# Performance work log

Measured on AMD Instinct MI355X. Metric: run time of the kernel, lower is better.

## Reference

```python
import jax, jax.numpy as jnp
import numpy as np

SPATIAL_SHAPES = np.array([[128, 128], [64, 64], [32, 32], [16, 16]], dtype=np.int32)  # (H, W) per level
D_MODEL = 256
D_FFN = 1024
N_LEVELS = 4
N_HEADS = 8
N_POINTS = 4
HEAD_DIM = D_MODEL // N_HEADS
B = 2
LEN = int((SPATIAL_SHAPES[:, 0] * SPATIAL_SHAPES[:, 1]).sum())  # 21760


def layer_norm(x, g, b, eps=1e-5):
    mu = x.mean(-1, keepdims=True)
    var = ((x - mu) ** 2).mean(-1, keepdims=True)
    return (x - mu) / jnp.sqrt(var + eps) * g + b


def ms_deform_attn_core(value, sampling_locations, attention_weights):
    # value: [B, Len, M, D]; locations: [B, Lq, M, L, P, 2] in [0,1]; weights: [B, Lq, M, L, P]
    B_, _, M, D = value.shape
    Lq = sampling_locations.shape[1]
    P = sampling_locations.shape[4]
    out = jnp.zeros((B_, M, Lq, D), value.dtype)
    start = 0
    for lvl, (H, W) in enumerate(SPATIAL_SHAPES.tolist()):
        v = value[:, start:start + H * W].transpose(0, 2, 1, 3)  # [B, M, H*W, D]
        start += H * W
        loc = sampling_locations[:, :, :, lvl].transpose(0, 2, 1, 3, 4)  # [B, M, Lq, P, 2]
        # grid_sample semantics: align_corners=False, padding_mode='zeros'
        x = loc[..., 0] * W - 0.5
        y = loc[..., 1] * H - 0.5
        x0 = jnp.floor(x)
        y0 = jnp.floor(y)
        wx = (x - x0)[..., None]
        wy = (y - y0)[..., None]

        def gather(xi, yi):
            valid = ((xi >= 0) & (xi < W) & (yi >= 0) & (yi < H)).astype(value.dtype)
            idx = (jnp.clip(yi, 0, H - 1) * W + jnp.clip(xi, 0, W - 1)).astype(jnp.int32)
            idx = idx.reshape(B_, M, Lq * P)
            g = jnp.take_along_axis(v, idx[..., None], axis=2).reshape(B_, M, Lq, P, D)
            return g * valid[..., None]

        v00 = gather(x0, y0)
        v01 = gather(x0 + 1, y0)
        v10 = gather(x0, y0 + 1)
        v11 = gather(x0 + 1, y0 + 1)
        samp = (v00 * (1 - wx) + v01 * wx) * (1 - wy) + (v10 * (1 - wx) + v11 * wx) * wy
        w_l = attention_weights[:, :, :, lvl].transpose(0, 2, 1, 3)  # [B, M, Lq, P]
        out = out + (samp * w_l[..., None]).sum(axis=3)
    return out.transpose(0, 2, 1, 3).reshape(B_, Lq, M * D)


def setup_inputs() -> dict:
    key = jax.random.key(0)
    ks = jax.random.split(key, 16)
    f32 = jnp.float32

    def lin(k, fan_in, fan_out, scale=None):
        s = scale if scale is not None else 1.0 / np.sqrt(fan_in)
        return jax.random.normal(k, (fan_in, fan_out), f32) * s

    starts = np.concatenate([[0], np.cumsum(SPATIAL_SHAPES[:, 0] * SPATIAL_SHAPES[:, 1])[:-1]]).astype(np.int32)
    inp = {
        "src": jax.random.normal(ks[0], (B, LEN, D_MODEL), f32),
        "pos": jax.random.normal(ks[1], (B, LEN, D_MODEL), f32),
        "reference_points": jax.random.uniform(ks[2], (B, LEN, N_LEVELS, 2), f32),
        "spatial_shapes": jnp.asarray(SPATIAL_SHAPES),
        "level_start_index": jnp.asarray(starts),
        "norm1_g": jnp.ones((D_MODEL,), f32), "norm1_b": jnp.zeros((D_MODEL,), f32),
        "norm2_g": jnp.ones((D_MODEL,), f32), "norm2_b": jnp.zeros((D_MODEL,), f32),
        "W_value": lin(ks[3], D_MODEL, D_MODEL), "b_value": jnp.zeros((D_MODEL,), f32),
        "W_off": lin(ks[4], D_MODEL, N_HEADS * N_LEVELS * N_POINTS * 2, scale=0.01),
        "b_off": jax.random.normal(ks[5], (N_HEADS * N_LEVELS * N_POINTS * 2,), f32) * 0.01,
        "W_attn": lin(ks[6], D_MODEL, N_HEADS * N_LEVELS * N_POINTS),
        "b_attn": jnp.zeros((N_HEADS * N_LEVELS * N_POINTS,), f32),
        "W_out": lin(ks[7], D_MODEL, D_MODEL), "b_out": jnp.zeros((D_MODEL,), f32),
        "W_ffn1": lin(ks[8], D_MODEL, D_FFN), "b_ffn1": jnp.zeros((D_FFN,), f32),
        "W_ffn2": lin(ks[9], D_FFN, D_MODEL), "b_ffn2": jnp.zeros((D_MODEL,), f32),
    }
    return inp


def reference(src, pos, reference_points, spatial_shapes, level_start_index,
              norm1_g, norm1_b, norm2_g, norm2_b,
              W_value, b_value, W_off, b_off, W_attn, b_attn, W_out, b_out,
              W_ffn1, b_ffn1, W_ffn2, b_ffn2):
    B_, Lq, C = src.shape
    # pre-norm deformable self-attention; NOTE: value path uses un-normed src (faithful to source)
    q = layer_norm(src, norm1_g, norm1_b) + pos
    value = (src @ W_value + b_value).reshape(B_, Lq, N_HEADS, HEAD_DIM)
    offsets = (q @ W_off + b_off).reshape(B_, Lq, N_HEADS, N_LEVELS, N_POINTS, 2)
    attn = jax.nn.softmax((q @ W_attn + b_attn).reshape(B_, Lq, N_HEADS, N_LEVELS * N_POINTS), axis=-1)
    attn = attn.reshape(B_, Lq, N_HEADS, N_LEVELS, N_POINTS)
    offset_normalizer = spatial_shapes[..., ::-1].astype(src.dtype)  # (W, H) per level
    loc = reference_points[:, :, None, :, None, :] + offsets / offset_normalizer[None, None, None, :, None, :]
    attn_out = ms_deform_attn_core(value, loc, attn) @ W_out + b_out
    src = src + attn_out
    h = layer_norm(src, norm2_g, norm2_b)
    h = jax.nn.gelu(h @ W_ffn1 + b_ffn1, approximate=False) @ W_ffn2 + b_ffn2
    return src + h
```

## Files before the change

kernel.cpp:

```cpp
#include <hip/hip_runtime.h>
#include <hip/hip_bf16.h>
#include <math.h>

#define LEN_TOT 21760
#define BATCH 2
#define MROWS (BATCH * LEN_TOT)
#define DMODEL 256
#define DFFN 1024

typedef unsigned short ushort_t;
typedef __attribute__((ext_vector_type(8))) short short8;
typedef __attribute__((ext_vector_type(4))) float floatx4;
typedef __attribute__((address_space(3))) ushort_t lds_us;
typedef __attribute__((address_space(1))) const ushort_t glb_us;

__device__ __forceinline__ ushort_t f2b(float f) {
    unsigned u = __float_as_uint(f);
    unsigned r = (u + 0x7FFFu + ((u >> 16) & 1u)) >> 16;
    return (ushort_t)r;
}

struct TP {
    const float* s[6];
    ushort_t*    d[6];
    int K[6];
    int N[6];
    int start[7];
};

__global__ __launch_bounds__(256) void transpose_convert(TP tp) {
    __shared__ float tile[32][33];
    int blk = blockIdx.x;
    int seg = 0;
    while (seg < 5 && blk >= tp.start[seg + 1]) seg++;
    int local = blk - tp.start[seg];
    int K = tp.K[seg], N = tp.N[seg];
    int tn = N >> 5;
    int k0 = (local / tn) << 5, n0 = (local % tn) << 5;
    int r = threadIdx.x >> 5, c = threadIdx.x & 31;
    const float* src = tp.s[seg];
    #pragma unroll
    for (int rr = r; rr < 32; rr += 8)
        tile[rr][c] = src[(size_t)(k0 + rr) * N + n0 + c];
    __syncthreads();
    ushort_t* dst = tp.d[seg];
    #pragma unroll
    for (int rr = r; rr < 32; rr += 8)
        dst[(size_t)(n0 + rr) * K + k0 + c] = f2b(tile[c][rr]);
}

__global__ __launch_bounds__(256) void ln_dual_kernel(
    const float* __restrict__ x, const float* __restrict__ g,
    const float* __restrict__ bb, const float* __restrict__ addv,
    ushort_t* __restrict__ y_bf, ushort_t* __restrict__ x_bf)
{
    int row  = blockIdx.x * 4 + (threadIdx.x >> 6);
    int lane = threadIdx.x & 63;
    size_t base = (size_t)row * DMODEL + lane * 4;
    float4 v = *(const float4*)(x + base);

    float s = v.x + v.y + v.z + v.w;
    #pragma unroll
    for (int o = 32; o; o >>= 1) s += __shfl_xor(s, o, 64);
    float mu = s * (1.0f / 256.0f);

    float d0 = v.x - mu, d1 = v.y - mu, d2 = v.z - mu, d3 = v.w - mu;
    float vs = d0*d0 + d1*d1 + d2*d2 + d3*d3;
    #pragma unroll
    for (int o = 32; o; o >>= 1) vs += __shfl_xor(vs, o, 64);
    float rstd = rsqrtf(vs * (1.0f / 256.0f) + 1e-5f);

    float4 gv = *(const float4*)(g  + lane * 4);
    float4 bv = *(const float4*)(bb + lane * 4);
    float o0 = d0 * rstd * gv.x + bv.x;
    float o1 = d1 * rstd * gv.y + bv.y;
    float o2 = d2 * rstd * gv.z + bv.z;
    float o3 = d3 * rstd * gv.w + bv.w;
    if (addv) {
        float4 av = *(const float4*)(addv + base);
        o0 += av.x; o1 += av.y; o2 += av.z; o3 += av.w;
    }
    ushort4 ob = {f2b(o0), f2b(o1), f2b(o2), f2b(o3)};
    *(ushort4*)(y_bf + base) = ob;
    if (x_bf) {
        ushort4 xb = {f2b(v.x), f2b(v.y), f2b(v.z), f2b(v.w)};
        *(ushort4*)(x_bf + base) = xb;
    }
}

template<int GELU_ACT, int HAS_RES, int OUT_BF16>
__global__ __launch_bounds__(256) void gemm_mfma(
    const ushort_t* __restrict__ A, const ushort_t* __restrict__ Bt,
    const float* __restrict__ bias, const float* __restrict__ res,
    float* __restrict__ C, ushort_t* __restrict__ Cbf,
    int M, int N, int K)
{
    constexpr int BM = 128, BK = 32;
    __shared__ __align__(16) ushort_t As[BM * BK];
    __shared__ __align__(16) ushort_t Bs[BM * BK];

    const int tid  = threadIdx.x;
    const int wave = tid >> 6;
    const int lane = tid & 63;
    const int wm = (wave & 1) * 64;
    const int wn = (wave >> 1) * 64;
    const int ml = lane & 15;
    const int quad = lane >> 4;
    const int m0 = blockIdx.y * BM, n0 = blockIdx.x * BM;

    const int r0 = tid >> 2, s0 = tid & 3;
    const int r1 = (tid + 256) >> 2;

    floatx4 acc[4][4] = {};

    for (int k0 = 0; k0 < K; k0 += BK) {
        const ushort_t* gA0 = A  + (size_t)(m0 + r0) * K + k0 + s0 * 8;
        const ushort_t* gA1 = A  + (size_t)(m0 + r1) * K + k0 + s0 * 8;
        const ushort_t* gB0 = Bt + (size_t)(n0 + r0) * K + k0 + s0 * 8;
        const ushort_t* gB1 = Bt + (size_t)(n0 + r1) * K + k0 + s0 * 8;
        __builtin_amdgcn_global_load_lds((glb_us*)gA0, (lds_us*)(As + tid * 8),        16, 0, 0);
        __builtin_amdgcn_global_load_lds((glb_us*)gA1, (lds_us*)(As + (tid + 256) * 8),16, 0, 0);
        __builtin_amdgcn_global_load_lds((glb_us*)gB0, (lds_us*)(Bs + tid * 8),        16, 0, 0);
        __builtin_amdgcn_global_load_lds((glb_us*)gB1, (lds_us*)(Bs + (tid + 256) * 8),16, 0, 0);
        __syncthreads();

        short8 af[4], bfr[4];
        #pragma unroll
        for (int i = 0; i < 4; i++)
            af[i] = *(const short8*)(As + (wm + i * 16 + ml) * BK + quad * 8);
        #pragma unroll
        for (int j = 0; j < 4; j++)
            bfr[j] = *(const short8*)(Bs + (wn + j * 16 + ml) * BK + quad * 8);
        #pragma unroll
        for (int i = 0; i < 4; i++)
            #pragma unroll
            for (int j = 0; j < 4; j++)
                acc[i][j] = __builtin_amdgcn_mfma_f32_16x16x32_bf16(
                    af[i], bfr[j], acc[i][j], 0, 0, 0);
        __syncthreads();
    }

    if (OUT_BF16) {
        ushort_t* pool  = (wave < 2) ? As : Bs;
        ushort_t* wbase = pool + (wave & 1) * 2048;
        const int lr  = lane >> 2;
        const int sg  = lane & 3;
        #pragma unroll
        for (int i = 0; i < 4; i++) {
            ushort_t* wbuf = wbase + (i & 1) * 1024;
            #pragma unroll
            for (int j = 0; j < 4; j++) {
                float bc = bias[n0 + wn + j * 16 + ml];
                #pragma unroll
                for (int r = 0; r < 4; r++) {
                    float v = acc[i][j][r] + bc;
                    if (GELU_ACT) v = 0.5f * v * (1.0f + erff(v * 0.7071067811865476f));
                    if (HAS_RES)
                        v += res[(size_t)(m0 + wm + i * 16 + quad * 4 + r) * N
                                 + n0 + wn + j * 16 + ml];
                    wbuf[(quad * 4 + r) * 64 + j * 16 + ml] = f2b(v);
                }
            }
            asm volatile("s_waitcnt lgkmcnt(0)" ::: "memory");
            #pragma unroll
            for (int h = 0; h < 2; h++) {
                short8 vv = *(const short8*)(wbuf + lr * 64 + (sg + 4 * h) * 8);
                *(short8*)(Cbf + (size_t)(m0 + wm + i * 16 + lr) * N
                                 + n0 + wn + (sg + 4 * h) * 8) = vv;
            }
        }
    } else {
        #pragma unroll
        for (int j = 0; j < 4; j++) {
            int col = n0 + wn + j * 16 + ml;
            float bc = bias[col];
            #pragma unroll
            for (int i = 0; i < 4; i++) {
                int row = m0 + wm + i * 16 + quad * 4;
                #pragma unroll
                for (int r = 0; r < 4; r++) {
                    float v = acc[i][j][r] + bc;
                    if (GELU_ACT) v = 0.5f * v * (1.0f + erff(v * 0.7071067811865476f));
                    if (HAS_RES) v += res[(size_t)(row + r) * N + col];
                    C[(size_t)(row + r) * N + col] = v;
                }
            }
        }
    }
}

__global__ __launch_bounds__(256) void msdeform_kernel(
    const float* __restrict__ value, const float* __restrict__ offs,
    const float* __restrict__ logits, const float* __restrict__ refp,
    ushort_t* __restrict__ out_bf)
{
    int gid = blockIdx.x * 8 + (threadIdx.x >> 5);
    int l   = threadIdx.x & 31;
    int bq  = gid >> 3;
    int m   = gid & 7;
    int b   = (bq >= LEN_TOT) ? 1 : 0;

    int i = l & 15;
    float logit = logits[(size_t)gid * 16 + i];
    float mx = logit;
    #pragma unroll
    for (int o = 8; o; o >>= 1) mx = fmaxf(mx, __shfl_xor(mx, o, 32));
    float e = __expf(logit - mx);
    float se = e;
    #pragma unroll
    for (int o = 8; o; o >>= 1) se += __shfl_xor(se, o, 32);
    float prob = e / se;

    int lvl = i >> 2;
    int Wl  = 128 >> lvl;
    float Wf = (float)Wl;
    const int ST_[4] = {0, 16384, 20480, 21504};

    float2 off2 = ((const float2*)offs)[(size_t)gid * 16 + i];
    float2 ref2 = ((const float2*)refp)[(size_t)bq * 4 + lvl];
    float xs = fmaf(ref2.x, Wf, off2.x) - 0.5f;
    float ys = fmaf(ref2.y, Wf, off2.y) - 0.5f;
    float xf = floorf(xs), yf = floorf(ys);
    int x0 = (int)xf, y0 = (int)yf;
    float wx = xs - xf, wy = ys - yf;
    float wx1 = 1.0f - wx, wy1 = 1.0f - wy;

    bool vx0 = (x0 >= 0) & (x0 < Wl);
    bool vx1 = (x0 + 1 >= 0) & (x0 + 1 < Wl);
    bool vy0 = (y0 >= 0) & (y0 < Wl);
    bool vy1 = (y0 + 1 >= 0) & (y0 + 1 < Wl);
    int cx0 = min(max(x0, 0), Wl - 1);
    int cx1 = min(max(x0 + 1, 0), Wl - 1);
    int cy0 = min(max(y0, 0), Wl - 1);
    int cy1 = min(max(y0 + 1, 0), Wl - 1);

    int vbase = b * LEN_TOT + ST_[lvl];
    int i00 = (vbase + cy0 * Wl + cx0) * 256 + m * 32;
    int i01 = (vbase + cy0 * Wl + cx1) * 256 + m * 32;
    int i10 = (vbase + cy1 * Wl + cx0) * 256 + m * 32;
    int i11 = (vbase + cy1 * Wl + cx1) * 256 + m * 32;
    float w00 = (vx0 && vy0) ? prob * wx1 * wy1 : 0.0f;
    float w01 = (vx1 && vy0) ? prob * wx  * wy1 : 0.0f;
    float w10 = (vx0 && vy1) ? prob * wx1 * wy  : 0.0f;
    float w11 = (vx1 && vy1) ? prob * wx  * wy  : 0.0f;

    int sA = l >> 2;
    int cA = l & 3;
    int t0 = __shfl(i00, sA, 32), t1 = __shfl(i01, sA, 32);
    int t2 = __shfl(i10, sA, 32), t3 = __shfl(i11, sA, 32);
    int addrA = (cA == 0) ? t0 : (cA == 1) ? t1 : (cA == 2) ? t2 : t3;
    float u0 = __shfl(w00, sA, 32), u1 = __shfl(w01, sA, 32);
    float u2 = __shfl(w10, sA, 32), u3 = __shfl(w11, sA, 32);
    float wA = (cA == 0) ? u0 : (cA == 1) ? u1 : (cA == 2) ? u2 : u3;
    t0 = __shfl(i00, sA + 8, 32); t1 = __shfl(i01, sA + 8, 32);
    t2 = __shfl(i10, sA + 8, 32); t3 = __shfl(i11, sA + 8, 32);
    int addrB = (cA == 0) ? t0 : (cA == 1) ? t1 : (cA == 2) ? t2 : t3;
    u0 = __shfl(w00, sA + 8, 32); u1 = __shfl(w01, sA + 8, 32);
    u2 = __shfl(w10, sA + 8, 32); u3 = __shfl(w11, sA + 8, 32);
    float wB = (cA == 0) ? u0 : (cA == 1) ? u1 : (cA == 2) ? u2 : u3;

    int cl = l >> 3;
    int d4 = l & 7;
    float ax = 0.0f, ay = 0.0f, az = 0.0f, aw = 0.0f;
    #pragma unroll
    for (int s = 0; s < 8; s++) {
        int   a = __shfl(addrA, s * 4 + cl, 32);
        float w = __shfl(wA,    s * 4 + cl, 32);
        float4 v = *(const float4*)(value + a + (d4 << 2));
        ax = fmaf(w, v.x, ax); ay = fmaf(w, v.y, ay);
        az = fmaf(w, v.z, az); aw = fmaf(w, v.w, aw);
    }
    #pragma unroll
    for (int s = 0; s < 8; s++) {
        int   a = __shfl(addrB, s * 4 + cl, 32);
        float w = __shfl(wB,    s * 4 + cl, 32);
        float4 v = *(const float4*)(value + a + (d4 << 2));
        ax = fmaf(w, v.x, ax); ay = fmaf(w, v.y, ay);
        az = fmaf(w, v.z, az); aw = fmaf(w, v.w, aw);
    }
    ax += __shfl_xor(ax, 8, 32);  ay += __shfl_xor(ay, 8, 32);
    az += __shfl_xor(az, 8, 32);  aw += __shfl_xor(aw, 8, 32);
    ax += __shfl_xor(ax, 16, 32); ay += __shfl_xor(ay, 16, 32);
    az += __shfl_xor(az, 16, 32); aw += __shfl_xor(aw, 16, 32);

    if (l < 8) {
        ushort4 o = {f2b(ax), f2b(ay), f2b(az), f2b(aw)};
        *(ushort4*)(out_bf + (size_t)gid * 32 + (d4 << 2)) = o;
    }
}

extern "C" void kernel_launch(void* const* d_in, const int* in_sizes, int n_in,
                              void* d_out, int out_size, void* d_ws, size_t ws_size,
                              hipStream_t stream)
{
    const float* src  = (const float*)d_in[0];
    const float* pos  = (const float*)d_in[1];
    const float* refp = (const float*)d_in[2];
    const float* n1g = (const float*)d_in[5];
    const float* n1b = (const float*)d_in[6];
    const float* n2g = (const float*)d_in[7];
    const float* n2b = (const float*)d_in[8];
    const float* Wv  = (const float*)d_in[9];
    const float* bv  = (const float*)d_in[10];
    const float* Wof = (const float*)d_in[11];
    const float* bof = (const float*)d_in[12];
    const float* Wat = (const float*)d_in[13];
    const float* bat = (const float*)d_in[14];
    const float* Wo  = (const float*)d_in[15];
    const float* bo  = (const float*)d_in[16];
    const float* Wf1 = (const float*)d_in[17];
    const float* bf1 = (const float*)d_in[18];
    const float* Wf2 = (const float*)d_in[19];
    const float* bf2 = (const float*)d_in[20];
    float* out = (float*)d_out;

    char* ws = (char*)d_ws;
    const int M = MROWS;
    const size_t SZ_BF = (size_t)M * 256 * 2;
    const size_t SZ_F  = (size_t)M * 256 * 4;

    ushort_t* q_bf    = (ushort_t*)(ws);
    float*    value   = (float*)   (ws + SZ_BF);
    ushort_t* src_bf  = (ushort_t*)(ws + SZ_BF + SZ_F);
    float*    offsb   = (float*)   (ws + 2 * SZ_BF + SZ_F);
    float*    logitsb = (float*)   (ws + 2 * SZ_BF + 2 * SZ_F);
    ushort_t* h0_bf   = q_bf;
    ushort_t* sampled = src_bf;
    float*    src2    = value;
    ushort_t* h1_bf   = src_bf;
    char* wtp = ws + 2 * SZ_BF + 2 * SZ_F + (size_t)M * 128 * 4;
    ushort_t* WvT  = (ushort_t*)(wtp);
    ushort_t* WofT = WvT  + 256 * 256;
    ushort_t* WatT = WofT + 256 * 256;
    ushort_t* WoT  = WatT + 256 * 128;
    ushort_t* Wf1T = WoT  + 256 * 256;
    ushort_t* Wf2T = Wf1T + 256 * 1024;

    TP tp;
    tp.s[0] = Wv;  tp.d[0] = WvT;  tp.K[0] = 256;  tp.N[0] = 256;
    tp.s[1] = Wof; tp.d[1] = WofT; tp.K[1] = 256;  tp.N[1] = 256;
    tp.s[2] = Wat; tp.d[2] = WatT; tp.K[2] = 256;  tp.N[2] = 128;
    tp.s[3] = Wo;  tp.d[3] = WoT;  tp.K[3] = 256;  tp.N[3] = 256;
    tp.s[4] = Wf1; tp.d[4] = Wf1T; tp.K[4] = 256;  tp.N[4] = 1024;
    tp.s[5] = Wf2; tp.d[5] = Wf2T; tp.K[5] = 1024; tp.N[5] = 256;
    tp.start[0] = 0;   tp.start[1] = 64;  tp.start[2] = 128;
    tp.start[3] = 160; tp.start[4] = 224; tp.start[5] = 480; tp.start[6] = 736;
    transpose_convert<<<736, 256, 0, stream>>>(tp);

    ln_dual_kernel<<<M / 4, 256, 0, stream>>>(src, n1g, n1b, pos, q_bf, src_bf);
    gemm_mfma<0, 0, 0><<<dim3(2, M / 128), 256, 0, stream>>>(
        src_bf, WvT, bv, nullptr, value, nullptr, M, 256, 256);
    gemm_mfma<0, 0, 0><<<dim3(2, M / 128), 256, 0, stream>>>(
        q_bf, WofT, bof, nullptr, offsb, nullptr, M, 256, 256);
    gemm_mfma<0, 0, 0><<<dim3(1, M / 128), 256, 0, stream>>>(
        q_bf, WatT, bat, nullptr, logitsb, nullptr, M, 128, 256);
    msdeform_kernel<<<M, 256, 0, stream>>>(value, offsb, logitsb, refp, sampled);
    gemm_mfma<0, 1, 0><<<dim3(2, M / 128), 256, 0, stream>>>(
        sampled, WoT, bo, src, src2, nullptr, M, 256, 256);
    ln_dual_kernel<<<M / 4, 256, 0, stream>>>(src2, n2g, n2b, nullptr, h0_bf, nullptr);
    gemm_mfma<1, 0, 1><<<dim3(8, M / 128), 256, 0, stream>>>(
        h0_bf, Wf1T, bf1, nullptr, nullptr, h1_bf, M, 1024, 256);
    gemm_mfma<0, 1, 0><<<dim3(2, M / 128), 256, 0, stream>>>(
        h1_bf, Wf2T, bf2, src2, out, nullptr, M, 256, 1024);
}
```

Baseline: 505.1 us.

## Use bf16 value, fuse offset/attn GEMMs, swizzle BK=64 GEMM, chunk FFN

The GEMM K-tile grows to 64, with an XOR-swizzled LDS layout meant to avoid bank conflicts. The value projection now writes bf16, and msdeform gathers bf16, which halves gather bandwidth. Offset and attention-logit GEMMs merge into one N=384 GEMM with concatenated biases. msdeform is restructured to one query per block, with sampling metadata staged in shared memory. The FFN runs in two row chunks so the intermediate buffer is smaller and more cache-friendly, at the cost of extra launches and bf16 rounding of the value tensor.

```diff
diff --git a/kernel.cpp b/kernel.cpp
--- a/kernel.cpp
+++ b/kernel.cpp
@@ -49,6 +49,12 @@
         dst[(size_t)(n0 + rr) * K + k0 + c] = f2b(tile[c][rr]);
 }
 
+__global__ void bias_cat(const float* __restrict__ a, const float* __restrict__ b,
+                         float* __restrict__ o) {
+    int t = threadIdx.x;
+    o[t] = (t < 256) ? a[t] : b[t - 256];
+}
+
 __global__ __launch_bounds__(256) void ln_dual_kernel(
     const float* __restrict__ x, const float* __restrict__ g,
     const float* __restrict__ bb, const float* __restrict__ addv,
@@ -95,7 +101,7 @@
     float* __restrict__ C, ushort_t* __restrict__ Cbf,
     int M, int N, int K)
 {
-    constexpr int BM = 128, BK = 32;
+    constexpr int BM = 128, BK = 64;
     __shared__ __align__(16) ushort_t As[BM * BK];
     __shared__ __align__(16) ushort_t Bs[BM * BK];
 
@@ -107,36 +113,42 @@
     const int ml = lane & 15;
     const int quad = lane >> 4;
     const int m0 = blockIdx.y * BM, n0 = blockIdx.x * BM;
-
-    const int r0 = tid >> 2, s0 = tid & 3;
-    const int r1 = (tid + 256) >> 2;
+    const int swz = ml & 7;
 
     floatx4 acc[4][4] = {};
 
     for (int k0 = 0; k0 < K; k0 += BK) {
-        const ushort_t* gA0 = A  + (size_t)(m0 + r0) * K + k0 + s0 * 8;
-        const ushort_t* gA1 = A  + (size_t)(m0 + r1) * K + k0 + s0 * 8;
-        const ushort_t* gB0 = Bt + (size_t)(n0 + r0) * K + k0 + s0 * 8;
-        const ushort_t* gB1 = Bt + (size_t)(n0 + r1) * K + k0 + s0 * 8;
-        __builtin_amdgcn_global_load_lds((glb_us*)gA0, (lds_us*)(As + tid * 8),        16, 0, 0);
-        __builtin_amdgcn_global_load_lds((glb_us*)gA1, (lds_us*)(As + (tid + 256) * 8),16, 0, 0);
-        __builtin_amdgcn_global_load_lds((glb_us*)gB0, (lds_us*)(Bs + tid * 8),        16, 0, 0);
-        __builtin_amdgcn_global_load_lds((glb_us*)gB1, (lds_us*)(Bs + (tid + 256) * 8),16, 0, 0);
+        #pragma unroll
+        for (int p = 0; p < 4; p++) {
+            int c = p * 256 + tid;
+            int r = c >> 3, sp = c & 7;
+            int sl = sp ^ (r & 7);
+            __builtin_amdgcn_global_load_lds(
+                (glb_us*)(A + (size_t)(m0 + r) * K + k0 + sl * 8),
+                (lds_us*)(As + c * 8), 16, 0, 0);
+            __builtin_amdgcn_global_load_lds(
+                (glb_us*)(Bt + (size_t)(n0 + r) * K + k0 + sl * 8),
+                (lds_us*)(Bs + c * 8), 16, 0, 0);
+        }
         __syncthreads();
 
-        short8 af[4], bfr[4];
-        #pragma unroll
-        for (int i = 0; i < 4; i++)
-            af[i] = *(const short8*)(As + (wm + i * 16 + ml) * BK + quad * 8);
-        #pragma unroll
-        for (int j = 0; j < 4; j++)
-            bfr[j] = *(const short8*)(Bs + (wn + j * 16 + ml) * BK + quad * 8);
-        #pragma unroll
-        for (int i = 0; i < 4; i++)
+        #pragma unroll
+        for (int kb = 0; kb < 2; kb++) {
+            const int sA = quad + 4 * kb;
+            short8 af[4], bfr[4];
+            #pragma unroll
+            for (int i = 0; i < 4; i++)
+                af[i] = *(const short8*)(As + (wm + i * 16 + ml) * BK + (sA ^ swz) * 8);
             #pragma unroll
             for (int j = 0; j < 4; j++)
-                acc[i][j] = __builtin_amdgcn_mfma_f32_16x16x32_bf16(
-                    af[i], bfr[j], acc[i][j], 0, 0, 0);
+                bfr[j] = *(const short8*)(Bs + (wn + j * 16 + ml) * BK + (sA ^ swz) * 8);
+            #pragma unroll
+            for (int i = 0; i < 4; i++)
+                #pragma unroll
+                for (int j = 0; j < 4; j++)
+                    acc[i][j] = __builtin_amdgcn_mfma_f32_16x16x32_bf16(
+                        af[i], bfr[j], acc[i][j], 0, 0, 0);
+        }
         __syncthreads();
     }
 
@@ -190,93 +202,83 @@
 }
 
 __global__ __launch_bounds__(256) void msdeform_kernel(
-    const float* __restrict__ value, const float* __restrict__ offs,
-    const float* __restrict__ logits, const float* __restrict__ refp,
-    ushort_t* __restrict__ out_bf)
+    const ushort_t* __restrict__ value, const float* __restrict__ qk,
+    const float* __restrict__ refp, ushort_t* __restrict__ out_bf)
 {
-    int gid = blockIdx.x * 8 + (threadIdx.x >> 5);
-    int l   = threadIdx.x & 31;
-    int bq  = gid >> 3;
-    int m   = gid & 7;
-    int b   = (bq >= LEN_TOT) ? 1 : 0;
-
-    int i = l & 15;
-    float logit = logits[(size_t)gid * 16 + i];
-    float mx = logit;
-    #pragma unroll
-    for (int o = 8; o; o >>= 1) mx = fmaxf(mx, __shfl_xor(mx, o, 32));
-    float e = __expf(logit - mx);
-    float se = e;
-    #pragma unroll
-    for (int o = 8; o; o >>= 1) se += __shfl_xor(se, o, 32);
-    float prob = e / se;
-
-    int lvl = i >> 2;
-    int Wl  = 128 >> lvl;
-    float Wf = (float)Wl;
-    const int ST_[4] = {0, 16384, 20480, 21504};
-
-    float2 off2 = ((const float2*)offs)[(size_t)gid * 16 + i];
-    float2 ref2 = ((const float2*)refp)[(size_t)bq * 4 + lvl];
-    float xs = fmaf(ref2.x, Wf, off2.x) - 0.5f;
-    float ys = fmaf(ref2.y, Wf, off2.y) - 0.5f;
-    float xf = floorf(xs), yf = floorf(ys);
-    int x0 = (int)xf, y0 = (int)yf;
-    float wx = xs - xf, wy = ys - yf;
-    float wx1 = 1.0f - wx, wy1 = 1.0f - wy;
-
-    bool vx0 = (x0 >= 0) & (x0 < Wl);
-    bool vx1 = (x0 + 1 >= 0) & (x0 + 1 < Wl);
-    bool vy0 = (y0 >= 0) & (y0 < Wl);
-    bool vy1 = (y0 + 1 >= 0) & (y0 + 1 < Wl);
-    int cx0 = min(max(x0, 0), Wl - 1);
-    int cx1 = min(max(x0 + 1, 0), Wl - 1);
-    int cy0 = min(max(y0, 0), Wl - 1);
-    int cy1 = min(max(y0 + 1, 0), Wl - 1);
-
-    int vbase = b * LEN_TOT + ST_[lvl];
-    int i00 = (vbase + cy0 * Wl + cx0) * 256 + m * 32;
-    int i01 = (vbase + cy0 * Wl + cx1) * 256 + m * 32;
-    int i10 = (vbase + cy1 * Wl + cx0) * 256 + m * 32;
-    int i11 = (vbase + cy1 * Wl + cx1) * 256 + m * 32;
-    float w00 = (vx0 && vy0) ? prob * wx1 * wy1 : 0.0f;
-    float w01 = (vx1 && vy0) ? prob * wx  * wy1 : 0.0f;
-    float w10 = (vx0 && vy1) ? prob * wx1 * wy  : 0.0f;
-    float w11 = (vx1 && vy1) ? prob * wx  * wy  : 0.0f;
-
-    int sA = l >> 2;
-    int cA = l & 3;
-    int t0 = __shfl(i00, sA, 32), t1 = __shfl(i01, sA, 32);
-    int t2 = __shfl(i10, sA, 32), t3 = __shfl(i11, sA, 32);
-    int addrA = (cA == 0) ? t0 : (cA == 1) ? t1 : (cA == 2) ? t2 : t3;
-    float u0 = __shfl(w00, sA, 32), u1 = __shfl(w01, sA, 32);
-    float u2 = __shfl(w10, sA, 32), u3 = __shfl(w11, sA, 32);
-    float wA = (cA == 0) ? u0 : (cA == 1) ? u1 : (cA == 2) ? u2 : u3;
-    t0 = __shfl(i00, sA + 8, 32); t1 = __shfl(i01, sA + 8, 32);
-    t2 = __shfl(i10, sA + 8, 32); t3 = __shfl(i11, sA + 8, 32);
-    int addrB = (cA == 0) ? t0 : (cA == 1) ? t1 : (cA == 2) ? t2 : t3;
-    u0 = __shfl(w00, sA + 8, 32); u1 = __shfl(w01, sA + 8, 32);
-    u2 = __shfl(w10, sA + 8, 32); u3 = __shfl(w11, sA + 8, 32);
-    float wB = (cA == 0) ? u0 : (cA == 1) ? u1 : (cA == 2) ? u2 : u3;
-
-    int cl = l >> 3;
-    int d4 = l & 7;
+    __shared__ int2 meta[8][16][4];
+
+    const int t  = threadIdx.x;
+    const int bq = blockIdx.x;
+    const int b  = (bq >= LEN_TOT) ? 1 : 0;
+
+    if (t < 128) {
+        int g = t >> 4, i = t & 15;
+        float logit = qk[(size_t)bq * 384 + 256 + g * 16 + i];
+        float mx = logit;
+        #pragma unroll
+        for (int o = 8; o; o >>= 1) mx = fmaxf(mx, __shfl_xor(mx, o, 16));
+        float e = __expf(logit - mx);
+        float se = e;
+        #pragma unroll
+        for (int o = 8; o; o >>= 1) se += __shfl_xor(se, o, 16);
+        float prob = e / se;
+
+        int lvl = i >> 2;
+        int Wl  = 128 >> lvl;
+        float Wf = (float)Wl;
+        const int ST_[4] = {0, 16384, 20480, 21504};
+
+        float2 off2 = *(const float2*)(qk + (size_t)bq * 384 + g * 32 + i * 2);
+        float2 ref2 = ((const float2*)refp)[(size_t)bq * 4 + lvl];
+        float xs = fmaf(ref2.x, Wf, off2.x) - 0.5f;
+        float ys = fmaf(ref2.y, Wf, off2.y) - 0.5f;
+        float xf = floorf(xs), yf = floorf(ys);
+        int x0 = (int)xf, y0 = (int)yf;
+        float wx = xs - xf, wy = ys - yf;
+        float wx1 = 1.0f - wx, wy1 = 1.0f - wy;
+
+        bool vx0 = (x0 >= 0) & (x0 < Wl);
+        bool vx1 = (x0 + 1 >= 0) & (x0 + 1 < Wl);
+        bool vy0 = (y0 >= 0) & (y0 < Wl);
+        bool vy1 = (y0 + 1 >= 0) & (y0 + 1 < Wl);
+        int cx0 = min(max(x0, 0), Wl - 1);
+        int cx1 = min(max(x0 + 1, 0), Wl - 1);
+        int cy0 = min(max(y0, 0), Wl - 1);
+        int cy1 = min(max(y0 + 1, 0), Wl - 1);
+
+        int vbase = b * LEN_TOT + ST_[lvl];
+        int i00 = (vbase + cy0 * Wl + cx0) * 256 + g * 32;
+        int i01 = (vbase + cy0 * Wl + cx1) * 256 + g * 32;
+        int i10 = (vbase + cy1 * Wl + cx0) * 256 + g * 32;
+        int i11 = (vbase + cy1 * Wl + cx1) * 256 + g * 32;
+        float w00 = (vx0 && vy0) ? prob * wx1 * wy1 : 0.0f;
+        float w01 = (vx1 && vy0) ? prob * wx  * wy1 : 0.0f;
+        float w10 = (vx0 && vy1) ? prob * wx1 * wy  : 0.0f;
+        float w11 = (vx1 && vy1) ? prob * wx  * wy  : 0.0f;
+
+        *(int4*)&meta[g][i][0] = make_int4(i00, __float_as_int(w00),
+                                           i01, __float_as_int(w01));
+        *(int4*)&meta[g][i][2] = make_int4(i10, __float_as_int(w10),
+                                           i11, __float_as_int(w11));
+    }
+    __syncthreads();
+
+    const int g  = t >> 5;
+    const int l  = t & 31;
+    const int cl = l >> 3;
+    const int d4 = l & 7;
     float ax = 0.0f, ay = 0.0f, az = 0.0f, aw = 0.0f;
     #pragma unroll
-    for (int s = 0; s < 8; s++) {
-        int   a = __shfl(addrA, s * 4 + cl, 32);
-        float w = __shfl(wA,    s * 4 + cl, 32);
-        float4 v = *(const float4*)(value + a + (d4 << 2));
-        ax = fmaf(w, v.x, ax); ay = fmaf(w, v.y, ay);
-        az = fmaf(w, v.z, az); aw = fmaf(w, v.w, aw);
-    }
-    #pragma unroll
-    for (int s = 0; s < 8; s++) {
-        int   a = __shfl(addrB, s * 4 + cl, 32);
-        float w = __shfl(wB,    s * 4 + cl, 32);
-        float4 v = *(const float4*)(value + a + (d4 << 2));
-        ax = fmaf(w, v.x, ax); ay = fmaf(w, v.y, ay);
-        az = fmaf(w, v.z, az); aw = fmaf(w, v.w, aw);
+    for (int s = 0; s < 16; s++) {
+        int2 mw = meta[g][s][cl];
+        float w = __int_as_float(mw.y);
+        uint2 u = *(const uint2*)(value + mw.x + (d4 << 2));
+        float f0 = __uint_as_float(u.x << 16);
+        float f1 = __uint_as_float(u.x & 0xFFFF0000u);
+        float f2 = __uint_as_float(u.y << 16);
+        float f3 = __uint_as_float(u.y & 0xFFFF0000u);
+        ax = fmaf(w, f0, ax); ay = fmaf(w, f1, ay);
+        az = fmaf(w, f2, az); aw = fmaf(w, f3, aw);
     }
     ax += __shfl_xor(ax, 8, 32);  ay += __shfl_xor(ay, 8, 32);
     az += __shfl_xor(az, 8, 32);  aw += __shfl_xor(aw, 8, 32);
@@ -285,7 +287,7 @@
 
     if (l < 8) {
         ushort4 o = {f2b(ax), f2b(ay), f2b(az), f2b(aw)};
-        *(ushort4*)(out_bf + (size_t)gid * 32 + (d4 << 2)) = o;
+        *(ushort4*)(out_bf + ((size_t)bq * 8 + g) * 32 + (d4 << 2)) = o;
     }
 }
 
@@ -315,26 +317,26 @@
     float* out = (float*)d_out;
 
     char* ws = (char*)d_ws;
-    const int M = MROWS;
+    const int M  = MROWS;
+    const int Mc = M / 2;
     const size_t SZ_BF = (size_t)M * 256 * 2;
-    const size_t SZ_F  = (size_t)M * 256 * 4;
-
-    ushort_t* q_bf    = (ushort_t*)(ws);
-    float*    value   = (float*)   (ws + SZ_BF);
-    ushort_t* src_bf  = (ushort_t*)(ws + SZ_BF + SZ_F);
-    float*    offsb   = (float*)   (ws + 2 * SZ_BF + SZ_F);
-    float*    logitsb = (float*)   (ws + 2 * SZ_BF + 2 * SZ_F);
-    ushort_t* h0_bf   = q_bf;
-    ushort_t* sampled = src_bf;
-    float*    src2    = value;
-    ushort_t* h1_bf   = src_bf;
-    char* wtp = ws + 2 * SZ_BF + 2 * SZ_F + (size_t)M * 128 * 4;
+
+    ushort_t* q_bf     = (ushort_t*)(ws);
+    ushort_t* src_bf   = (ushort_t*)(ws + SZ_BF);
+    ushort_t* value_bf = (ushort_t*)(ws + 2 * SZ_BF);
+    float*    qkb      = (float*)   (ws + 3 * SZ_BF);
+    float*    src2     = (float*)   (ws + 4 * SZ_BF);
+    ushort_t* h0_bf    = q_bf;
+    ushort_t* sampled  = src_bf;
+    ushort_t* h1_bf    = value_bf;
+    char* wtp = ws + 3 * SZ_BF + (size_t)M * 384 * 4;
     ushort_t* WvT  = (ushort_t*)(wtp);
     ushort_t* WofT = WvT  + 256 * 256;
     ushort_t* WatT = WofT + 256 * 256;
     ushort_t* WoT  = WatT + 256 * 128;
     ushort_t* Wf1T = WoT  + 256 * 256;
     ushort_t* Wf2T = Wf1T + 256 * 1024;
+    float*    bqk  = (float*)(Wf2T + 1024 * 256);
 
     TP tp;
     tp.s[0] = Wv;  tp.d[0] = WvT;  tp.K[0] = 256;  tp.N[0] = 256;
@@ -346,20 +348,24 @@
     tp.start[0] = 0;   tp.start[1] = 64;  tp.start[2] = 128;
     tp.start[3] = 160; tp.start[4] = 224; tp.start[5] = 480; tp.start[6] = 736;
     transpose_convert<<<736, 256, 0, stream>>>(tp);
+    bias_cat<<<1, 384, 0, stream>>>(bof, bat, bqk);
 
     ln_dual_kernel<<<M / 4, 256, 0, stream>>>(src, n1g, n1b, pos, q_bf, src_bf);
-    gemm_mfma<0, 0, 0><<<dim3(2, M / 128), 256, 0, stream>>>(
-        src_bf, WvT, bv, nullptr, value, nullptr, M, 256, 256);
-    gemm_mfma<0, 0, 0><<<dim3(2, M / 128), 256, 0, stream>>>(
-        q_bf, WofT, bof, nullptr, offsb, nullptr, M, 256, 256);
-    gemm_mfma<0, 0, 0><<<dim3(1, M / 128), 256, 0, stream>>>(
-        q_bf, WatT, bat, nullptr, logitsb, nullptr, M, 128, 256);
-    msdeform_kernel<<<M, 256, 0, stream>>>(value, offsb, logitsb, refp, sampled);
+    gemm_mfma<0, 0, 1><<<dim3(2, M / 128), 256, 0, stream>>>(
+        src_bf, WvT, bv, nullptr, nullptr, value_bf, M, 256, 256);
+    gemm_mfma<0, 0, 0><<<dim3(3, M / 128), 256, 0, stream>>>(
+        q_bf, WofT, bqk, nullptr, qkb, nullptr, M, 384, 256);
+    msdeform_kernel<<<M, 256, 0, stream>>>(value_bf, qkb, refp, sampled);
     gemm_mfma<0, 1, 0><<<dim3(2, M / 128), 256, 0, stream>>>(
         sampled, WoT, bo, src, src2, nullptr, M, 256, 256);
     ln_dual_kernel<<<M / 4, 256, 0, stream>>>(src2, n2g, n2b, nullptr, h0_bf, nullptr);
-    gemm_mfma<1, 0, 1><<<dim3(8, M / 128), 256, 0, stream>>>(
-        h0_bf, Wf1T, bf1, nullptr, nullptr, h1_bf, M, 1024, 256);
-    gemm_mfma<0, 1, 0><<<dim3(2, M / 128), 256, 0, stream>>>(
-        h1_bf, Wf2T, bf2, src2, out, nullptr, M, 256, 1024);
-}
+    for (int c = 0; c < 2; c++) {
+        const ushort_t* h0c = h0_bf + (size_t)c * Mc * 256;
+        const float*    s2c = src2  + (size_t)c * Mc * 256;
+        float*          oc  = out   + (size_t)c * Mc * 256;
+        gemm_mfma<1, 0, 1><<<dim3(8, Mc / 128), 256, 0, stream>>>(
+            h0c, Wf1T, bf1, nullptr, nullptr, h1_bf, Mc, 1024, 256);
+        gemm_mfma<0, 1, 0><<<dim3(2, Mc / 128), 256, 0, stream>>>(
+            h1_bf, Wf2T, bf2, s2c, oc, nullptr, Mc, 256, 1024);
+    }
+}
```

Measured after the change: 505.4 us. Within noise of the previous version (+0.1%).
